# Optimization experiments

Hardware: AMD Instinct MI355X
Metric: run time of the kernel (lower is better)

## Reference

```python
import jax, jax.numpy as jnp
import numpy as np

N, C, D = 32768, 1000, 512


def setup_inputs() -> dict:
    key = jax.random.key(0)
    k1, k2, k3, k4 = jax.random.split(key, 4)
    features = jax.random.normal(k1, (N, D), dtype=jnp.float32)
    labels = jax.random.randint(k2, (N,), 0, C, dtype=jnp.int64)
    # center as built in __init__: randn(C, D) * |normal(1, 2, (C, 1))|
    weight = jnp.abs(1.0 + 2.0 * jax.random.normal(k3, (C, 1), dtype=jnp.float32))
    center = jax.random.normal(k4, (C, D), dtype=jnp.float32) * weight
    return {"features": features, "labels": labels, "center": center}


def reference(features, labels, center):
    # Original: dist_mat = cdist(features, center, p=2); mask = one_hot(labels);
    # loss = sum(dist_mat * mask) / N.
    # Since the mask is one-hot over classes and distances are >= 0, the masked
    # row-sum equals the L2 distance to the true-class center, so we gather the
    # correct center per sample instead of materializing the [N, C] cdist matrix.
    # This is numerically identical math (same sqrt-of-sum-of-squares per pair).
    c = jax.lax.stop_gradient(center)  # intra_loss detaches the center
    diff = features - c[labels]                      # [N, D]
    dist = jnp.sqrt(jnp.sum(diff * diff, axis=1))    # [N]
    return jnp.sum(dist) / features.shape[0]
```

## Files before the change

kernel.cpp:

```cpp
#include <hip/hip_runtime.h>


#define GRID  1024
#define BLOCK 256

__global__ __launch_bounds__(BLOCK) void intra_partial(
    const float* __restrict__ features,
    const int*   __restrict__ labels,
    const float* __restrict__ center,
    float*       __restrict__ partial)
{
    const int lane  = threadIdx.x & 63;
    const int wid   = threadIdx.x >> 6;
    const int gwave = blockIdx.x * 4 + wid;

    float acc = 0.0f;

    #pragma unroll
    for (int k = 0; k < 8; ++k) {
        const int row = gwave + k * 4096;
        const int lbl = labels[row];
        const float4* f = reinterpret_cast<const float4*>(features + (size_t)row * 512);
        const float4* c = reinterpret_cast<const float4*>(center   + (size_t)lbl * 512);

        float ss = 0.0f;
        #pragma unroll
        for (int p = 0; p < 2; ++p) {
            const float4 fv = f[p * 64 + lane];
            const float4 cv = c[p * 64 + lane];
            const float dx = fv.x - cv.x;
            const float dy = fv.y - cv.y;
            const float dz = fv.z - cv.z;
            const float dw = fv.w - cv.w;
            ss += dx * dx + dy * dy + dz * dz + dw * dw;
        }

        #pragma unroll
        for (int off = 32; off > 0; off >>= 1)
            ss += __shfl_down(ss, off, 64);

        if (lane == 0)
            acc += sqrtf(ss);
    }

    __shared__ float s[4];
    if (lane == 0) s[wid] = acc;
    __syncthreads();
    if (threadIdx.x == 0)
        partial[blockIdx.x] = s[0] + s[1] + s[2] + s[3];
}

__global__ __launch_bounds__(1024) void final_reduce(
    const float* __restrict__ partial,
    float*       __restrict__ out)
{
    float v = partial[threadIdx.x];

    #pragma unroll
    for (int off = 32; off > 0; off >>= 1)
        v += __shfl_down(v, off, 64);

    __shared__ float s[16];
    if ((threadIdx.x & 63) == 0) s[threadIdx.x >> 6] = v;
    __syncthreads();
    if (threadIdx.x == 0) {
        float t = 0.0f;
        #pragma unroll
        for (int i = 0; i < 16; ++i) t += s[i];
        *out = t * (1.0f / 32768.0f);
    }
}

extern "C" void kernel_launch(void* const* d_in, const int* in_sizes, int n_in,
                              void* d_out, int out_size, void* d_ws, size_t ws_size,
                              hipStream_t stream) {
    const float* features = (const float*)d_in[0];
    const int*   labels   = (const int*)d_in[1];
    const float* center   = (const float*)d_in[2];
    float* out     = (float*)d_out;
    float* partial = (float*)d_ws;

    intra_partial<<<GRID, BLOCK, 0, stream>>>(features, labels, center, partial);
    final_reduce<<<1, 1024, 0, stream>>>(partial, out);
}
```

Measured before the change: 97.65 us.

## Raise grid to 4096 blocks, two rows per wave with nontemporal feature loads

```diff
diff --git a/kernel.cpp b/kernel.cpp
--- a/kernel.cpp
+++ b/kernel.cpp
@@ -1,10 +1,12 @@
 #include <hip/hip_runtime.h>
 
 
-#define GRID  1024
+typedef float f32x4 __attribute__((ext_vector_type(4)));
+
+#define GRID  4096
 #define BLOCK 256
 
-__global__ __launch_bounds__(BLOCK) void intra_partial(
+__global__ __launch_bounds__(BLOCK, 8) void intra_partial(
     const float* __restrict__ features,
     const int*   __restrict__ labels,
     const float* __restrict__ center,
@@ -14,37 +16,41 @@
     const int wid   = threadIdx.x >> 6;
     const int gwave = blockIdx.x * 4 + wid;
 
-    float acc = 0.0f;
+    const int r0 = gwave;
+    const int r1 = gwave + 16384;
+
+    const int l0 = labels[r0];
+    const int l1 = labels[r1];
+
+    const f32x4* f0 = (const f32x4*)(features + (size_t)r0 * 512);
+    const f32x4* f1 = (const f32x4*)(features + (size_t)r1 * 512);
+    const f32x4 fa0 = __builtin_nontemporal_load(f0 + lane);
+    const f32x4 fb0 = __builtin_nontemporal_load(f0 + 64 + lane);
+    const f32x4 fa1 = __builtin_nontemporal_load(f1 + lane);
+    const f32x4 fb1 = __builtin_nontemporal_load(f1 + 64 + lane);
+
+    const f32x4* c0 = (const f32x4*)(center + (size_t)l0 * 512);
+    const f32x4* c1 = (const f32x4*)(center + (size_t)l1 * 512);
+    const f32x4 ca0 = c0[lane];
+    const f32x4 cb0 = c0[64 + lane];
+    const f32x4 ca1 = c1[lane];
+    const f32x4 cb1 = c1[64 + lane];
+
+    f32x4 d;
+    float ss0, ss1;
+    d = fa0 - ca0; ss0  = d.x * d.x + d.y * d.y + d.z * d.z + d.w * d.w;
+    d = fb0 - cb0; ss0 += d.x * d.x + d.y * d.y + d.z * d.z + d.w * d.w;
+    d = fa1 - ca1; ss1  = d.x * d.x + d.y * d.y + d.z * d.z + d.w * d.w;
+    d = fb1 - cb1; ss1 += d.x * d.x + d.y * d.y + d.z * d.z + d.w * d.w;
 
     #pragma unroll
-    for (int k = 0; k < 8; ++k) {
-        const int row = gwave + k * 4096;
-        const int lbl = labels[row];
-        const float4* f = reinterpret_cast<const float4*>(features + (size_t)row * 512);
-        const float4* c = reinterpret_cast<const float4*>(center   + (size_t)lbl * 512);
-
-        float ss = 0.0f;
-        #pragma unroll
-        for (int p = 0; p < 2; ++p) {
-            const float4 fv = f[p * 64 + lane];
-            const float4 cv = c[p * 64 + lane];
-            const float dx = fv.x - cv.x;
-            const float dy = fv.y - cv.y;
-            const float dz = fv.z - cv.z;
-            const float dw = fv.w - cv.w;
-            ss += dx * dx + dy * dy + dz * dz + dw * dw;
-        }
-
-        #pragma unroll
-        for (int off = 32; off > 0; off >>= 1)
-            ss += __shfl_down(ss, off, 64);
-
-        if (lane == 0)
-            acc += sqrtf(ss);
+    for (int off = 32; off > 0; off >>= 1) {
+        ss0 += __shfl_down(ss0, off, 64);
+        ss1 += __shfl_down(ss1, off, 64);
     }
 
     __shared__ float s[4];
-    if (lane == 0) s[wid] = acc;
+    if (lane == 0) s[wid] = sqrtf(ss0) + sqrtf(ss1);
     __syncthreads();
     if (threadIdx.x == 0)
         partial[blockIdx.x] = s[0] + s[1] + s[2] + s[3];
@@ -54,7 +60,10 @@
     const float* __restrict__ partial,
     float*       __restrict__ out)
 {
-    float v = partial[threadIdx.x];
+    float v = partial[threadIdx.x]
+            + partial[threadIdx.x + 1024]
+            + partial[threadIdx.x + 2048]
+            + partial[threadIdx.x + 3072];
 
     #pragma unroll
     for (int off = 32; off > 0; off >>= 1)
```

Result: slower. 102.9 us (+5.4%).
